# Performance work log

Hardware: AMD Instinct MI355X
Metric: run time of the kernel (lower is better)

The kernel has to match this reference:

```python
import jax, jax.numpy as jnp
import numpy as np

H = 16          # num_attention_heads
HD = 64         # hidden_size_per_attention_head
EPS = 1e-12

def _layernorm(x, w, b):
    u = x.mean(-1, keepdims=True)
    s = ((x - u) ** 2).mean(-1, keepdims=True)
    return w * (x - u) / jnp.sqrt(s + EPS) + b

def _split_heads(x):
    b, s, d = x.shape
    return x.reshape(b, s, H, d // H).transpose(0, 2, 1, 3)  # [b,h,s,hd]

def _merge_heads(x):
    b, h, s, hd = x.shape
    return x.transpose(0, 2, 1, 3).reshape(b, s, h * hd)


def setup_inputs() -> dict:
    key = jax.random.key(0)
    ks = jax.random.split(key, 20)
    B, S, T, D, F = 4, 1024, 1024, 1024, 4096
    w = lambda k, shp: (jax.random.normal(k, shp, jnp.float32) * 0.02)
    return {
        "hidden_states": jax.random.normal(ks[0], (B, S, D), jnp.float32),
        "enc_hidden_states": jax.random.normal(ks[1], (B, T, D), jnp.float32),
        "enc_attn_mask": jnp.zeros((B, 1, 1, T), jnp.float32),
        "dec_attn_mask": jnp.tril(jnp.ones((S, S), jnp.float32)).reshape(1, 1, S, S),
        "ln1_w": jnp.ones((D,), jnp.float32), "ln1_b": jnp.zeros((D,), jnp.float32),
        "qkv_w": w(ks[2], (D, 3 * D)), "qkv_b": jnp.zeros((3 * D,), jnp.float32),
        "attn_o_w": w(ks[3], (D, D)), "attn_o_b": jnp.zeros((D,), jnp.float32),
        "ln2_w": jnp.ones((D,), jnp.float32), "ln2_b": jnp.zeros((D,), jnp.float32),
        "q_w": w(ks[4], (D, D)), "q_b": jnp.zeros((D,), jnp.float32),
        "kv_w": w(ks[5], (D, 2 * D)), "kv_b": jnp.zeros((2 * D,), jnp.float32),
        "ca_o_w": w(ks[6], (D, D)), "ca_o_b": jnp.zeros((D,), jnp.float32),
        "ln3_w": jnp.ones((D,), jnp.float32), "ln3_b": jnp.zeros((D,), jnp.float32),
        "ffn_in_w": w(ks[7], (D, F)), "ffn_in_b": jnp.zeros((F,), jnp.float32),
        "ffn_out_w": w(ks[8], (F, D)), "ffn_out_b": jnp.zeros((D,), jnp.float32),
    }


def reference(hidden_states, enc_hidden_states, enc_attn_mask, dec_attn_mask,
              ln1_w, ln1_b, qkv_w, qkv_b, attn_o_w, attn_o_b,
              ln2_w, ln2_b, q_w, q_b, kv_w, kv_b, ca_o_w, ca_o_b,
              ln3_w, ln3_b, ffn_in_w, ffn_in_b, ffn_out_w, ffn_out_b):
    scale = 1.0 / jnp.sqrt(jnp.float32(HD))
    # dropout layers are identity (eval mode)

    # ---- self-attention (ltor multiplicative mask formula) ----
    residual = hidden_states
    x = _layernorm(hidden_states, ln1_w, ln1_b)
    qkv = x @ qkv_w + qkv_b
    q, k, v = jnp.split(qkv, 3, axis=-1)
    q, k, v = _split_heads(q), _split_heads(k), _split_heads(v)
    scores = jnp.einsum('bhsd,bhtd->bhst', q, k) * scale
    scores = scores * dec_attn_mask - 10000.0 * (1.0 - dec_attn_mask)
    probs = jax.nn.softmax(scores, axis=-1)
    ctx = _merge_heads(jnp.einsum('bhst,bhtd->bhsd', probs, v))
    hidden_states = residual + (ctx @ attn_o_w + attn_o_b)

    # ---- cross-attention (additive enc mask) ----
    residual = hidden_states
    x = _layernorm(hidden_states, ln2_w, ln2_b)
    q = _split_heads(x @ q_w + q_b)
    kv = enc_hidden_states @ kv_w + kv_b
    k, v = jnp.split(kv, 2, axis=-1)
    k, v = _split_heads(k), _split_heads(v)
    scores = jnp.einsum('bhsd,bhtd->bhst', q, k) * scale + enc_attn_mask
    probs = jax.nn.softmax(scores, axis=-1)
    ctx = _merge_heads(jnp.einsum('bhst,bhtd->bhsd', probs, v))
    hidden_states = residual + (ctx @ ca_o_w + ca_o_b)

    # ---- FFN ----
    residual = hidden_states
    x = _layernorm(hidden_states, ln3_w, ln3_b)
    x = jax.nn.gelu(x @ ffn_in_w + ffn_in_b, approximate=False)
    x = x @ ffn_out_w + ffn_out_b
    return residual + x
```

## Files before the change

kernel.cpp:

```cpp
#include <hip/hip_runtime.h>
#include <cstdint>
#include <cstddef>

typedef unsigned short u16;
typedef __bf16 bf16x8 __attribute__((ext_vector_type(8)));
typedef float f32x4 __attribute__((ext_vector_type(4)));

__device__ __forceinline__ u16 f2bf(float f) {
  unsigned u = __float_as_uint(f);
  u += 0x7fffu + ((u >> 16) & 1u);
  return (u16)(u >> 16);
}

__device__ __forceinline__ float block_sum(float v, float* sbuf, int tid) {
#pragma unroll
  for (int off = 1; off < 64; off <<= 1) v += __shfl_xor(v, off, 64);
  if ((tid & 63) == 0) sbuf[tid >> 6] = v;
  __syncthreads();
  v = sbuf[0] + sbuf[1] + sbuf[2] + sbuf[3];
  __syncthreads();
  return v;
}

__device__ __forceinline__ void gld16(const void* g, void* l) {
  __builtin_amdgcn_global_load_lds((const __attribute__((address_space(1))) void*)g,
                                   (__attribute__((address_space(3))) void*)l,
                                   16, 0, 0);
}



#define BIG_PREAMBLE(BM, Kdim, KB)                                               \
  constexpr int NQA = (BM) / 64;                                                 \
  constexpr int IF  = (BM) / 32;                                                 \
  const int tid = threadIdx.x;                                                   \
  const int lane = tid & 63, wave = tid >> 6;                                    \
  const int l15 = lane & 15, g = (lane >> 4) & 3;                                \
  const int wr = (wave >> 2) * ((BM) / 2), wc = (wave & 3) * 64;                 \
  const int gx = gridDim.x;                                                      \
  const int nwg = gx * gridDim.y;                                                \
  const int id = blockIdx.y * gx + blockIdx.x;                                   \
  const int qq = nwg >> 3, rr = nwg & 7;                                         \
  const int xcd = id & 7, slot = id >> 3;                                        \
  const int sid = (xcd < rr ? xcd * (qq + 1) : rr * (qq + 1) + (xcd - rr) * qq) + slot; \
  const int bx = sid % gx, by = sid / gx;                                        \
  const int m0 = by * (BM), n0 = bx * 256;                                       \
  size_t aoff[NQA]; int adst[NQA];                                               \
  size_t boff[4];   int bdst[4];                                                 \
  _Pragma("unroll")                                                              \
  for (int q = 0; q < NQA; ++q) {                                                \
    const int c = tid + q * 512, row = c >> 3, ch = (c & 7) ^ (row & 7);         \
    aoff[q] = (size_t)(m0 + row) * (Kdim) + ch * 8 + (KB);                       \
    adst[q] = c * 8;                                                             \
  }                                                                              \
  _Pragma("unroll")                                                              \
  for (int q = 0; q < 4; ++q) {                                                  \
    const int c = tid + q * 512, row = c >> 3, ch = (c & 7) ^ (row & 7);         \
    boff[q] = (size_t)(n0 + row) * (Kdim) + ch * 8 + (KB);                       \
    bdst[q] = c * 8;                                                             \
  }

#define BIG_STAGE(BM, kk, buf)                                                   \
  {                                                                              \
    _Pragma("unroll")                                                            \
    for (int q = 0; q < NQA; ++q) gld16(A + aoff[q] + (kk), As + (buf) * ((BM) * 64) + adst[q]); \
    _Pragma("unroll")                                                            \
    for (int q = 0; q < 4; ++q)  gld16(B + boff[q] + (kk), Bs + (buf) * 16384 + bdst[q]); \
  }

#define BIG_COMPUTE(BM, buf)                                                     \
  {                                                                              \
    _Pragma("unroll")                                                            \
    for (int ks = 0; ks < 2; ++ks) {                                             \
      const int chR = (((ks * 4 + g) ^ (l15 & 7)) * 8);                          \
      bf16x8 af[IF], bg[4];                                                      \
      _Pragma("unroll")                                                          \
      for (int i = 0; i < IF; ++i)                                               \
        af[i] = *(const bf16x8*)(As + (buf) * ((BM) * 64) + (wr + i * 16 + l15) * 64 + chR); \
      _Pragma("unroll")                                                          \
      for (int j = 0; j < 4; ++j)                                                \
        bg[j] = *(const bf16x8*)(Bs + (buf) * 16384 + (wc + j * 16 + l15) * 64 + chR); \
      _Pragma("unroll")                                                          \
      for (int i = 0; i < IF; ++i)                                               \
        _Pragma("unroll")                                                        \
        for (int j = 0; j < 4; ++j)                                              \
          acc[i][j] = __builtin_amdgcn_mfma_f32_16x16x32_bf16(af[i], bg[j], acc[i][j], 0, 0, 0); \
    }                                                                            \
  }

#define BIG_WAIT_PREV(BM)                                                        \
  if constexpr ((BM) == 256)      asm volatile("s_waitcnt vmcnt(8)\ns_barrier" ::: "memory"); \
  else if constexpr ((BM) == 128) asm volatile("s_waitcnt vmcnt(6)\ns_barrier" ::: "memory"); \
  else                            asm volatile("s_waitcnt vmcnt(5)\ns_barrier" ::: "memory");

#define BIG_KLOOP(BM, NT)                                                        \
  f32x4 acc[IF][4] = {};                                                         \
  BIG_STAGE(BM, 0, 0)                                                            \
  int cur = 0;                                                                   \
  for (int t = 0; t < (NT) - 1; ++t) {                                           \
    BIG_STAGE(BM, (t + 1) * 64, cur ^ 1)                                         \
    BIG_WAIT_PREV(BM)                                                            \
    BIG_COMPUTE(BM, cur)                                                         \
    asm volatile("s_waitcnt lgkmcnt(0)\ns_barrier" ::: "memory");                \
    cur ^= 1;                                                                    \
  }                                                                              \
  asm volatile("s_waitcnt vmcnt(0)\ns_barrier" ::: "memory");                    \
  BIG_COMPUTE(BM, cur)

template<int BM, int MODE>
__global__ __launch_bounds__(512, 2) void gemm_big(
    const u16* __restrict__ A, const u16* __restrict__ B,
    const float* __restrict__ bias,
    u16* __restrict__ out0, u16* __restrict__ out1, u16* __restrict__ out2,
    int N, int K)
{
  __shared__ __align__(16) u16 As[2 * BM * 64];
  __shared__ __align__(16) u16 Bs[2 * 256 * 64];
  BIG_PREAMBLE(BM, K, 0)
  const int NT = K >> 6;
  BIG_KLOOP(BM, NT)

  if constexpr (MODE == 0) {
#pragma unroll
    for (int i = 0; i < IF; ++i) {
#pragma unroll
      for (int j = 0; j < 4; ++j) {
        const int col = n0 + wc + j * 16 + l15;
        const float bs = bias[col];
#pragma unroll
        for (int r = 0; r < 4; ++r) {
          const int gm = m0 + wr + i * 16 + g * 4 + r;
          float v = acc[i][j][r] + bs;
          v = 0.5f * v * (1.0f + erff(v * 0.70710678118654752f));
          out0[(size_t)gm * N + col] = f2bf(v);
        }
      }
    }
  } else {
#pragma unroll
    for (int i = 0; i < IF; ++i) {
#pragma unroll
      for (int j = 0; j < 4; ++j) {
        const int col = n0 + wc + j * 16 + l15;
        const int sec = (n0 + wc + j * 16) >> 10;
        const int tgt = (MODE == 1) ? sec : sec + 1;
        const float bs = bias[col];
#pragma unroll
        for (int r = 0; r < 4; ++r) {
          const int gm = m0 + wr + i * 16 + g * 4 + r;
          const float v = acc[i][j][r] + bs;
          const int cl = col & 1023, h = cl >> 6, d = cl & 63;
          const int z = (gm >> 10) * 16 + h, s = gm & 1023;
          if (tgt == 0)
            out0[((size_t)z * 1024 + s) * 64 + d] = f2bf(v * 0.125f);
          else if (tgt == 1)
            out1[((((size_t)z * 8 + (s >> 7)) * 8 + (d >> 3)) * 128 + (s & 127)) * 8 + (d & 7)] = f2bf(v);
          else
            out2[((size_t)z * 8 + (s >> 7)) * 8192 + (((s >> 3) & 15) * 64 + d) * 8 + (s & 7)] = f2bf(v);
        }
      }
    }
  }
}

template<int BM>
__global__ __launch_bounds__(512, 2) void gemm_part(
    const u16* __restrict__ A, const u16* __restrict__ B,
    float* __restrict__ part, int K, int Klen)
{
  __shared__ __align__(16) u16 As[2 * BM * 64];
  __shared__ __align__(16) u16 Bs[2 * 256 * 64];
  const int kb = blockIdx.z * Klen;
  float* outP = part + (size_t)blockIdx.z * (4096ULL * 1024);
  BIG_PREAMBLE(BM, K, kb)
  const int NT = Klen >> 6;
  BIG_KLOOP(BM, NT)

#pragma unroll
  for (int i = 0; i < IF; ++i)
#pragma unroll
    for (int j = 0; j < 4; ++j) {
      const int col = n0 + wc + j * 16 + l15;
#pragma unroll
      for (int r = 0; r < 4; ++r) {
        const int gm = m0 + wr + i * 16 + g * 4 + r;
        outP[(size_t)gm * 1024 + col] = acc[i][j][r];
      }
    }
}

__global__ __launch_bounds__(256, 4) void flash_attn(
    const u16* __restrict__ qh, const u16* __restrict__ kt, const u16* __restrict__ vt,
    const float* __restrict__ emask, u16* __restrict__ ctx, int causal)
{
  __shared__ __align__(16) u16 sK[8192];
  __shared__ __align__(16) u16 sV[8192];
  __shared__ __align__(16) u16 sP[64 * 64];

  const int tid = threadIdx.x, lane = tid & 63, wave = tid >> 6;
  const int l15 = lane & 15, g = (lane >> 4) & 3;
  const int id = blockIdx.y * 8 + blockIdx.x;
  const int xcd = id & 7, slot = id >> 3;
  const int z = xcd * 8 + (slot >> 4), b = z >> 4, h = z & 15;
  const int q0 = (slot & 15) * 64;
  const int r0 = wave * 16;
  const int qrel = q0 & 64;

  bf16x8 qf[2];
  {
    const u16* qz = qh + ((size_t)z * 1024 + q0 + r0 + l15) * 64 + g * 8;
#pragma unroll
    for (int kc = 0; kc < 2; ++kc)
      qf[kc] = *(const bf16x8*)(qz + kc * 32);
  }

  float m_i[4], l_i[4];
#pragma unroll
  for (int r = 0; r < 4; ++r) { m_i[r] = -1.0e30f; l_i[r] = 0.0f; }

  f32x4 o[4] = {};
  const int dt = (q0 >> 7) << 7;
  const int tmax = causal ? dt : 896;

  for (int t0 = 0; t0 <= tmax; t0 += 128) {
    const u16* ktile = kt + ((size_t)z * 8 + (t0 >> 7)) * 8192;
    const u16* vtile = vt + ((size_t)z * 8 + (t0 >> 7)) * 8192;
    __syncthreads();
#pragma unroll
    for (int i = 0; i < 4; ++i) {
      const int off = (wave * 4 + i) * 512 + lane * 8;
      gld16(ktile + off, sK + off);
      gld16(vtile + off, sV + off);
    }
    __syncthreads();

#pragma unroll
    for (int ci = 0; ci < 2; ++ci) {
      if (causal && t0 == dt && ci * 64 > qrel + r0 + 15) continue;

      f32x4 sa[4] = {};
#pragma unroll
      for (int kc = 0; kc < 2; ++kc) {
        bf16x8 bg[4];
#pragma unroll
        for (int jn = 0; jn < 4; ++jn)
          bg[jn] = *(const bf16x8*)(sK + ((kc * 4 + g) * 128 + ci * 64 + jn * 16 + l15) * 8);
#pragma unroll
        for (int jn = 0; jn < 4; ++jn)
          sa[jn] = __builtin_amdgcn_mfma_f32_16x16x32_bf16(qf[kc], bg[jn], sa[jn], 0, 0, 0);
      }

      if (causal) {
        if (t0 == dt && ci * 64 + 63 > qrel + r0) {
#pragma unroll
          for (int jn = 0; jn < 4; ++jn) {
            const int col = ci * 64 + jn * 16 + l15;
#pragma unroll
            for (int r = 0; r < 4; ++r) {
              const int row = qrel + r0 + g * 4 + r;
              if (col > row) sa[jn][r] = -3.0e38f;
            }
          }
        }
      } else {
#pragma unroll
        for (int jn = 0; jn < 4; ++jn) {
          const float mv = emask[(size_t)b * 1024 + t0 + ci * 64 + jn * 16 + l15];
#pragma unroll
          for (int r = 0; r < 4; ++r) sa[jn][r] += mv;
        }
      }

      float alpha[4];
#pragma unroll
      for (int r = 0; r < 4; ++r) {
        const int rowl = r0 + g * 4 + r;
        const int swzr = (rowl & 7) << 4;
        float v = fmaxf(fmaxf(sa[0][r], sa[1][r]), fmaxf(sa[2][r], sa[3][r]));
        v = fmaxf(v, __shfl_xor(v, 1, 64));
        v = fmaxf(v, __shfl_xor(v, 2, 64));
        v = fmaxf(v, __shfl_xor(v, 4, 64));
        v = fmaxf(v, __shfl_xor(v, 8, 64));
        const float mo = m_i[r];
        const float mn = fmaxf(mo, v);
        m_i[r] = mn;
        alpha[r] = __expf(mo - mn);
        float s = 0.0f;
#pragma unroll
        for (int jn = 0; jn < 4; ++jn) {
          const float p = __expf(sa[jn][r] - mn);
          s += p;
          sP[(rowl * 128 + ((jn * 32 + 2 * l15) ^ swzr)) >> 1] = f2bf(p);
        }
        s += __shfl_xor(s, 1, 64);
        s += __shfl_xor(s, 2, 64);
        s += __shfl_xor(s, 4, 64);
        s += __shfl_xor(s, 8, 64);
        l_i[r] = alpha[r] * l_i[r] + s;
      }

#pragma unroll
      for (int jn = 0; jn < 4; ++jn)
#pragma unroll
        for (int r = 0; r < 4; ++r)
          o[jn][r] *= alpha[r];

      asm volatile("s_waitcnt lgkmcnt(0)" ::: "memory");
#pragma unroll
      for (int kc2 = 0; kc2 < 2; ++kc2) {
        bf16x8 pa, vb[4];
        pa = *(const bf16x8*)(sP + (((r0 + l15) * 128 + ((kc2 * 64 + g * 16) ^ ((l15 & 7) << 4))) >> 1));
#pragma unroll
        for (int jn = 0; jn < 4; ++jn)
          vb[jn] = *(const bf16x8*)(sV + ((ci * 8 + kc2 * 4 + g) * 64 + jn * 16 + l15) * 8);
#pragma unroll
        for (int jn = 0; jn < 4; ++jn)
          o[jn] = __builtin_amdgcn_mfma_f32_16x16x32_bf16(pa, vb[jn], o[jn], 0, 0, 0);
      }
    }
  }

#pragma unroll
  for (int r = 0; r < 4; ++r) {
    const float inv = 1.0f / l_i[r];
    const size_t base = ((size_t)(b * 1024 + q0 + r0 + g * 4 + r)) * 1024 + h * 64;
#pragma unroll
    for (int jn = 0; jn < 4; ++jn)
      ctx[base + jn * 16 + l15] = f2bf(o[jn][r] * inv);
  }
}

struct PrepArgs {
  const float* w[7]; u16* wt[7]; int K[7]; int N[7]; int cum[7];
  const float* enc; u16* enc_bf;
  const float* hid; const float* ln1w; const float* ln1b; u16* xln;
};
__global__ __launch_bounds__(256) void prep_kernel(PrepArgs a) {
  __shared__ float t[32][33];
  __shared__ float sbuf[4];
  const int bb = blockIdx.x, tid = threadIdx.x;
  if (bb < 16384) {
    int wi = 0;
#pragma unroll
    for (int i = 0; i < 7; ++i) if (bb >= a.cum[i]) wi = i + 1; else break;
    const int base = wi ? a.cum[wi - 1] : 0;
    const int tileIdx = bb - base;
    const int Kd = a.K[wi], Nd = a.N[wi], nx = Nd >> 5;
    const int n0 = (tileIdx % nx) * 32, k0 = (tileIdx / nx) * 32;
    const float* w = a.w[wi]; u16* wt = a.wt[wi];
    const int tx = tid & 31, ty = tid >> 5;
#pragma unroll
    for (int r = ty; r < 32; r += 8) t[r][tx] = w[(size_t)(k0 + r) * Nd + n0 + tx];
    __syncthreads();
#pragma unroll
    for (int r = ty; r < 32; r += 8) wt[(size_t)(n0 + r) * Kd + k0 + tx] = f2bf(t[tx][r]);
  } else if (bb < 20480) {
    const size_t i = ((size_t)(bb - 16384) * 256 + tid) * 4;
    const float4 v = *(const float4*)(a.enc + i);
    ushort4 o; o.x = f2bf(v.x); o.y = f2bf(v.y); o.z = f2bf(v.z); o.w = f2bf(v.w);
    *(ushort4*)(a.enc_bf + i) = o;
  } else {
    const int row = bb - 20480;
    const float4 v = *(const float4*)(a.hid + (size_t)row * 1024 + tid * 4);
    float s = block_sum(v.x + v.y + v.z + v.w, sbuf, tid);
    const float u = s * (1.0f / 1024.0f);
    const float d0 = v.x - u, d1 = v.y - u, d2 = v.z - u, d3 = v.w - u;
    float sq = block_sum(d0 * d0 + d1 * d1 + d2 * d2 + d3 * d3, sbuf, tid);
    const float rstd = rsqrtf(sq * (1.0f / 1024.0f) + 1e-12f);
    const int c = tid * 4;
    ushort4 o;
    o.x = f2bf(a.ln1w[c + 0] * d0 * rstd + a.ln1b[c + 0]);
    o.y = f2bf(a.ln1w[c + 1] * d1 * rstd + a.ln1b[c + 1]);
    o.z = f2bf(a.ln1w[c + 2] * d2 * rstd + a.ln1b[c + 2]);
    o.w = f2bf(a.ln1w[c + 3] * d3 * rstd + a.ln1b[c + 3]);
    *(ushort4*)(a.xln + (size_t)row * 1024 + c) = o;
  }
}

__global__ __launch_bounds__(256) void ln_red1_kernel(
    const float* __restrict__ p0,
    const float* __restrict__ bias, const float* __restrict__ res,
    const float* __restrict__ w, const float* __restrict__ b,
    float* __restrict__ hOut, u16* __restrict__ xln)
{
  __shared__ float sbuf[4];
  const int row = blockIdx.x, tid = threadIdx.x;
  const size_t off = (size_t)row * 1024 + tid * 4;
  const int c = tid * 4;
  const float4 a0 = *(const float4*)(p0 + off);
  const float4 bs = *(const float4*)(bias + c);
  const float4 rs = *(const float4*)(res + off);
  float4 v;
  v.x = a0.x + bs.x + rs.x;
  v.y = a0.y + bs.y + rs.y;
  v.z = a0.z + bs.z + rs.z;
  v.w = a0.w + bs.w + rs.w;
  *(float4*)(hOut + off) = v;
  float s = block_sum(v.x + v.y + v.z + v.w, sbuf, tid);
  const float u = s * (1.0f / 1024.0f);
  const float d0 = v.x - u, d1 = v.y - u, d2 = v.z - u, d3 = v.w - u;
  float sq = block_sum(d0 * d0 + d1 * d1 + d2 * d2 + d3 * d3, sbuf, tid);
  const float rstd = rsqrtf(sq * (1.0f / 1024.0f) + 1e-12f);
  ushort4 o;
  o.x = f2bf(w[c + 0] * d0 * rstd + b[c + 0]);
  o.y = f2bf(w[c + 1] * d1 * rstd + b[c + 1]);
  o.z = f2bf(w[c + 2] * d2 * rstd + b[c + 2]);
  o.w = f2bf(w[c + 3] * d3 * rstd + b[c + 3]);
  *(ushort4*)(xln + off) = o;
}

__global__ __launch_bounds__(256) void reduce_q1_kernel(
    const float* __restrict__ p0,
    const float* __restrict__ bias, u16* __restrict__ qh)
{
  const int m = blockIdx.x, tid = threadIdx.x;
  const size_t off = (size_t)m * 1024 + tid * 4;
  const int n = tid * 4, h = n >> 6, d = n & 63;
  const int b = m >> 10, s = m & 1023;
  const float4 a0 = *(const float4*)(p0 + off);
  const float4 bs = *(const float4*)(bias + n);
  ushort4 o;
  o.x = f2bf((a0.x + bs.x) * 0.125f);
  o.y = f2bf((a0.y + bs.y) * 0.125f);
  o.z = f2bf((a0.z + bs.z) * 0.125f);
  o.w = f2bf((a0.w + bs.w) * 0.125f);
  *(ushort4*)(qh + ((size_t)((b * 16 + h) * 1024 + s)) * 64 + d) = o;
}

__global__ __launch_bounds__(256) void reduce_out_kernel(
    const float* __restrict__ p0, const float* __restrict__ p1,
    const float* __restrict__ bias, const float* __restrict__ res,
    float* __restrict__ out)
{
  const int m = blockIdx.x, tid = threadIdx.x;
  const size_t off = (size_t)m * 1024 + tid * 4;
  const int c = tid * 4;
  const float4 a0 = *(const float4*)(p0 + off);
  const float4 a1 = *(const float4*)(p1 + off);
  const float4 bs = *(const float4*)(bias + c);
  const float4 rs = *(const float4*)(res + off);
  float4 v;
  v.x = a0.x + a1.x + bs.x + rs.x;
  v.y = a0.y + a1.y + bs.y + rs.y;
  v.z = a0.z + a1.z + bs.z + rs.z;
  v.w = a0.w + a1.w + bs.w + rs.w;
  *(float4*)(out + off) = v;
}

constexpr size_t MB = 1024ULL * 1024;
constexpr size_t WT_QKV    = 0;
constexpr size_t WT_ATTN_O = 6 * MB;
constexpr size_t WT_Q      = 8 * MB;
constexpr size_t WT_KV     = 10 * MB;
constexpr size_t WT_CA_O   = 14 * MB;
constexpr size_t WT_FFN_IN = 16 * MB;
constexpr size_t WT_FFN_OUT= 24 * MB;
constexpr size_t ENC_BF    = 32 * MB;
constexpr size_t XLN       = 40 * MB;
constexpr size_t QH        = 48 * MB;
constexpr size_t KT        = 56 * MB;
constexpr size_t VT        = 64 * MB;
constexpr size_t CTX       = 72 * MB;
constexpr size_t HBUF      = 80 * MB;
constexpr size_t SP0       = 96 * MB;
constexpr size_t SP1       = 112 * MB;
constexpr size_t FFN_MID   = 128 * MB;

extern "C" void kernel_launch(void* const* d_in, const int* in_sizes, int n_in,
                              void* d_out, int out_size, void* d_ws, size_t ws_size,
                              hipStream_t stream) {
  const float* hidden   = (const float*)d_in[0];
  const float* enc      = (const float*)d_in[1];
  const float* encm     = (const float*)d_in[2];
  const float* ln1w = (const float*)d_in[4],  *ln1b = (const float*)d_in[5];
  const float* qkv_w = (const float*)d_in[6], *qkv_b = (const float*)d_in[7];
  const float* attn_o_w = (const float*)d_in[8], *attn_o_b = (const float*)d_in[9];
  const float* ln2w = (const float*)d_in[10], *ln2b = (const float*)d_in[11];
  const float* q_w = (const float*)d_in[12],  *q_b = (const float*)d_in[13];
  const float* kv_w = (const float*)d_in[14], *kv_b = (const float*)d_in[15];
  const float* ca_o_w = (const float*)d_in[16], *ca_o_b = (const float*)d_in[17];
  const float* ln3w = (const float*)d_in[18], *ln3b = (const float*)d_in[19];
  const float* ffn_in_w = (const float*)d_in[20], *ffn_in_b = (const float*)d_in[21];
  const float* ffn_out_w = (const float*)d_in[22], *ffn_out_b = (const float*)d_in[23];

  char* ws = (char*)d_ws;
  u16* wt_qkv    = (u16*)(ws + WT_QKV);
  u16* wt_attn_o = (u16*)(ws + WT_ATTN_O);
  u16* wt_q      = (u16*)(ws + WT_Q);
  u16* wt_kv     = (u16*)(ws + WT_KV);
  u16* wt_ca_o   = (u16*)(ws + WT_CA_O);
  u16* wt_ffn_in = (u16*)(ws + WT_FFN_IN);
  u16* wt_ffn_out= (u16*)(ws + WT_FFN_OUT);
  u16* enc_bf = (u16*)(ws + ENC_BF);
  u16* xln    = (u16*)(ws + XLN);
  u16* qh     = (u16*)(ws + QH);
  u16* kt     = (u16*)(ws + KT);
  u16* vt     = (u16*)(ws + VT);
  u16* ctx    = (u16*)(ws + CTX);
  float* hF   = (float*)(ws + HBUF);
  float* sp0  = (float*)(ws + SP0);
  float* sp1  = (float*)(ws + SP1);
  u16* ffn_mid = (u16*)(ws + FFN_MID);

  PrepArgs pa;
  pa.w[0] = qkv_w;    pa.wt[0] = wt_qkv;     pa.K[0] = 1024; pa.N[0] = 3072; pa.cum[0] = 3072;
  pa.w[1] = attn_o_w; pa.wt[1] = wt_attn_o;  pa.K[1] = 1024; pa.N[1] = 1024; pa.cum[1] = 4096;
  pa.w[2] = q_w;      pa.wt[2] = wt_q;       pa.K[2] = 1024; pa.N[2] = 1024; pa.cum[2] = 5120;
  pa.w[3] = kv_w;     pa.wt[3] = wt_kv;      pa.K[3] = 1024; pa.N[3] = 2048; pa.cum[3] = 7168;
  pa.w[4] = ca_o_w;   pa.wt[4] = wt_ca_o;    pa.K[4] = 1024; pa.N[4] = 1024; pa.cum[4] = 8192;
  pa.w[5] = ffn_in_w; pa.wt[5] = wt_ffn_in;  pa.K[5] = 1024; pa.N[5] = 4096; pa.cum[5] = 12288;
  pa.w[6] = ffn_out_w;pa.wt[6] = wt_ffn_out; pa.K[6] = 4096; pa.N[6] = 1024; pa.cum[6] = 16384;
  pa.enc = enc; pa.enc_bf = enc_bf;
  pa.hid = hidden; pa.ln1w = ln1w; pa.ln1b = ln1b; pa.xln = xln;
  prep_kernel<<<24576, 256, 0, stream>>>(pa);

  gemm_big<256, 1><<<dim3(12, 16), 512, 0, stream>>>(xln, wt_qkv, qkv_b, qh, kt, vt, 3072, 1024);
  flash_attn<<<dim3(8, 128), 256, 0, stream>>>(qh, kt, vt, nullptr, ctx, 1);
  gemm_part<64><<<dim3(4, 64, 1), 512, 0, stream>>>(ctx, wt_attn_o, sp0, 1024, 1024);
  ln_red1_kernel<<<4096, 256, 0, stream>>>(sp0, attn_o_b, hidden, ln2w, ln2b, hF, xln);

  gemm_part<64><<<dim3(4, 64, 1), 512, 0, stream>>>(xln, wt_q, sp0, 1024, 1024);
  reduce_q1_kernel<<<4096, 256, 0, stream>>>(sp0, q_b, qh);
  gemm_big<128, 3><<<dim3(8, 32), 512, 0, stream>>>(enc_bf, wt_kv, kv_b, nullptr, kt, vt, 2048, 1024);
  flash_attn<<<dim3(8, 128), 256, 0, stream>>>(qh, kt, vt, encm, ctx, 0);
  gemm_part<64><<<dim3(4, 64, 1), 512, 0, stream>>>(ctx, wt_ca_o, sp0, 1024, 1024);
  ln_red1_kernel<<<4096, 256, 0, stream>>>(sp0, ca_o_b, hF, ln3w, ln3b, hF, xln);

  gemm_big<256, 0><<<dim3(16, 16), 512, 0, stream>>>(xln, wt_ffn_in, ffn_in_b, ffn_mid, nullptr, nullptr, 4096, 1024);
  gemm_part<128><<<dim3(4, 32, 2), 512, 0, stream>>>(ffn_mid, wt_ffn_out, sp0, 4096, 2048);
  reduce_out_kernel<<<4096, 256, 0, stream>>>(sp0, sp1, ffn_out_b, hF, (float*)d_out);
}
```

Baseline: 558.2 us.

## Transpose QK^T MFMA layout and add lazy softmax rescaling in flash attention

Swaps the MFMA operands so each lane holds one query row's scores across key positions. The row max and sum then need only two cross-lane shuffles instead of four per row, and P can be written to shared memory as packed bf16x4 stores. It also adds a conditional online-softmax rescale that skips updating the running max and accumulators unless the new max exceeds the old one by more than 8. The encoder mask becomes a vector load, and P now uses native bf16 conversion instead of manual rounding. Skipping small max increases lets unnormalized exponentials grow by up to e^8, which is fine in fp32 but slightly changes rounding.

New measurement: 521.0 us. -6.7%, faster.

```diff
diff --git a/kernel.cpp b/kernel.cpp
--- a/kernel.cpp
+++ b/kernel.cpp
@@ -4,6 +4,7 @@
 
 typedef unsigned short u16;
 typedef __bf16 bf16x8 __attribute__((ext_vector_type(8)));
+typedef __bf16 bf16x4 __attribute__((ext_vector_type(4)));
 typedef float f32x4 __attribute__((ext_vector_type(4)));
 
 __device__ __forceinline__ u16 f2bf(float f) {
@@ -205,6 +206,7 @@
   const int q0 = (slot & 15) * 64;
   const int r0 = wave * 16;
   const int qrel = q0 & 64;
+  const int swzP = (l15 & 7) << 4;
 
   bf16x8 qf[2];
   {
@@ -214,10 +216,7 @@
       qf[kc] = *(const bf16x8*)(qz + kc * 32);
   }
 
-  float m_i[4], l_i[4];
-#pragma unroll
-  for (int r = 0; r < 4; ++r) { m_i[r] = -1.0e30f; l_i[r] = 0.0f; }
-
+  float m_i = -1.0e30f, l_i = 0.0f;
   f32x4 o[4] = {};
   const int dt = (q0 >> 7) << 7;
   const int tmax = causal ? dt : 896;
@@ -247,69 +246,80 @@
           bg[jn] = *(const bf16x8*)(sK + ((kc * 4 + g) * 128 + ci * 64 + jn * 16 + l15) * 8);
 #pragma unroll
         for (int jn = 0; jn < 4; ++jn)
-          sa[jn] = __builtin_amdgcn_mfma_f32_16x16x32_bf16(qf[kc], bg[jn], sa[jn], 0, 0, 0);
+          sa[jn] = __builtin_amdgcn_mfma_f32_16x16x32_bf16(bg[jn], qf[kc], sa[jn], 0, 0, 0);
       }
 
       if (causal) {
         if (t0 == dt && ci * 64 + 63 > qrel + r0) {
+          const int qq = qrel + r0 + l15;
 #pragma unroll
           for (int jn = 0; jn < 4; ++jn) {
-            const int col = ci * 64 + jn * 16 + l15;
 #pragma unroll
             for (int r = 0; r < 4; ++r) {
-              const int row = qrel + r0 + g * 4 + r;
-              if (col > row) sa[jn][r] = -3.0e38f;
+              const int trel = ci * 64 + jn * 16 + g * 4 + r;
+              if (trel > qq) sa[jn][r] = -3.0e38f;
             }
           }
         }
       } else {
 #pragma unroll
         for (int jn = 0; jn < 4; ++jn) {
-          const float mv = emask[(size_t)b * 1024 + t0 + ci * 64 + jn * 16 + l15];
-#pragma unroll
-          for (int r = 0; r < 4; ++r) sa[jn][r] += mv;
+          const f32x4 me = *(const f32x4*)(emask + (size_t)b * 1024 + t0 + ci * 64 + jn * 16 + g * 4);
+#pragma unroll
+          for (int r = 0; r < 4; ++r) sa[jn][r] += me[r];
         }
       }
 
-      float alpha[4];
-#pragma unroll
-      for (int r = 0; r < 4; ++r) {
-        const int rowl = r0 + g * 4 + r;
-        const int swzr = (rowl & 7) << 4;
-        float v = fmaxf(fmaxf(sa[0][r], sa[1][r]), fmaxf(sa[2][r], sa[3][r]));
-        v = fmaxf(v, __shfl_xor(v, 1, 64));
-        v = fmaxf(v, __shfl_xor(v, 2, 64));
-        v = fmaxf(v, __shfl_xor(v, 4, 64));
-        v = fmaxf(v, __shfl_xor(v, 8, 64));
-        const float mo = m_i[r];
-        const float mn = fmaxf(mo, v);
-        m_i[r] = mn;
-        alpha[r] = __expf(mo - mn);
-        float s = 0.0f;
-#pragma unroll
-        for (int jn = 0; jn < 4; ++jn) {
-          const float p = __expf(sa[jn][r] - mn);
-          s += p;
-          sP[(rowl * 128 + ((jn * 32 + 2 * l15) ^ swzr)) >> 1] = f2bf(p);
+      f32x4 m4;
+#pragma unroll
+      for (int r = 0; r < 4; ++r)
+        m4[r] = fmaxf(fmaxf(sa[0][r], sa[1][r]), fmaxf(sa[2][r], sa[3][r]));
+      float pmax = fmaxf(fmaxf(m4[0], m4[1]), fmaxf(m4[2], m4[3]));
+      pmax = fmaxf(pmax, __shfl_xor(pmax, 16, 64));
+      pmax = fmaxf(pmax, __shfl_xor(pmax, 32, 64));
+
+      if (!__all(pmax <= m_i + 8.0f)) {
+        const float mn = fmaxf(m_i, pmax);
+        const float al = __expf(m_i - mn);
+        m_i = mn;
+        l_i *= al;
+#pragma unroll
+        for (int r = 0; r < 4; ++r) {
+          const float ar = __shfl(al, g * 4 + r, 16);
+#pragma unroll
+          for (int jn = 0; jn < 4; ++jn) o[jn][r] *= ar;
         }
-        s += __shfl_xor(s, 1, 64);
-        s += __shfl_xor(s, 2, 64);
-        s += __shfl_xor(s, 4, 64);
-        s += __shfl_xor(s, 8, 64);
-        l_i[r] = alpha[r] * l_i[r] + s;
-      }
-
+      }
+
+      f32x4 p[4];
 #pragma unroll
       for (int jn = 0; jn < 4; ++jn)
 #pragma unroll
         for (int r = 0; r < 4; ++r)
-          o[jn][r] *= alpha[r];
+          p[jn][r] = __expf(sa[jn][r] - m_i);
+      f32x4 s4;
+#pragma unroll
+      for (int r = 0; r < 4; ++r)
+        s4[r] = (p[0][r] + p[1][r]) + (p[2][r] + p[3][r]);
+      float s = (s4[0] + s4[1]) + (s4[2] + s4[3]);
+      s += __shfl_xor(s, 16, 64);
+      s += __shfl_xor(s, 32, 64);
+      l_i += s;
+
+#pragma unroll
+      for (int jn = 0; jn < 4; ++jn) {
+        bf16x4 pk;
+#pragma unroll
+        for (int r = 0; r < 4; ++r) pk[r] = (__bf16)p[jn][r];
+        *(bf16x4*)(sP + (((r0 + l15) * 128 + ((jn * 32 + g * 8) ^ swzP)) >> 1)) = pk;
+      }
 
       asm volatile("s_waitcnt lgkmcnt(0)" ::: "memory");
+
 #pragma unroll
       for (int kc2 = 0; kc2 < 2; ++kc2) {
-        bf16x8 pa, vb[4];
-        pa = *(const bf16x8*)(sP + (((r0 + l15) * 128 + ((kc2 * 64 + g * 16) ^ ((l15 & 7) << 4))) >> 1));
+        const bf16x8 pa = *(const bf16x8*)(sP + (((r0 + l15) * 128 + ((kc2 * 64 + g * 16) ^ swzP)) >> 1));
+        bf16x8 vb[4];
 #pragma unroll
         for (int jn = 0; jn < 4; ++jn)
           vb[jn] = *(const bf16x8*)(sV + ((ci * 8 + kc2 * 4 + g) * 64 + jn * 16 + l15) * 8);
@@ -322,7 +332,7 @@
 
 #pragma unroll
   for (int r = 0; r < 4; ++r) {
-    const float inv = 1.0f / l_i[r];
+    const float inv = 1.0f / __shfl(l_i, g * 4 + r, 16);
     const size_t base = ((size_t)(b * 1024 + q0 + r0 + g * 4 + r)) * 1024 + h * 64;
 #pragma unroll
     for (int jn = 0; jn < 4; ++jn)
```
